# Kernel tuning notes

Hardware: AMD Instinct MI355X
Metric: run time of the kernel (lower is better)

Reference implementation:

```python
import jax, jax.numpy as jnp
import numpy as np

B, T, H = 4, 2048, 1024
NH, NKV, HD = 16, 4, 64  # heads, kv heads, head_dim

def setup_inputs() -> dict:
    key = jax.random.key(0)
    ks = jax.random.split(key, 5)
    s = 0.02
    return {
        "x": jax.random.normal(ks[0], (B, T, H), dtype=jnp.float32),
        "wq": jax.random.normal(ks[1], (H, NH * HD), dtype=jnp.float32) * s,
        "wk": jax.random.normal(ks[2], (H, NKV * HD), dtype=jnp.float32) * s,
        "wv": jax.random.normal(ks[3], (H, NKV * HD), dtype=jnp.float32) * s,
        "wo": jax.random.normal(ks[4], (NH * HD, H), dtype=jnp.float32) * s,
    }

def reference(x, wq, wk, wv, wo):
    b, t, _ = x.shape
    q = (x @ wq).reshape(b, t, NH, HD).transpose(0, 2, 1, 3)    # [B,NH,T,HD]
    k = (x @ wk).reshape(b, t, NKV, HD).transpose(0, 2, 1, 3)   # [B,NKV,T,HD]
    v = (x @ wv).reshape(b, t, NKV, HD).transpose(0, 2, 1, 3)
    n_rep = NH // NKV
    # repeat_kv: expand each kv head n_rep times along the head axis
    k_rep = jnp.repeat(k, n_rep, axis=1)                        # [B,NH,T,HD]
    v_rep = jnp.repeat(v, n_rep, axis=1)
    scale = 1.0 / np.sqrt(HD).astype(np.float32)
    scores = jnp.einsum('bhqd,bhkd->bhqk', q, k_rep) * scale    # [B,NH,T,T]
    key_pos = jnp.arange(t)[None, :]
    q_pos = jnp.arange(t)[:, None]  # past_len = 0 (no kv cache)
    causal = key_pos > q_pos                                    # [T,T]
    scores = jnp.where(causal[None, None], -jnp.inf, scores)
    probs = jax.nn.softmax(scores, axis=-1)                     # dropout is identity (eval / rate 0)
    attn = jnp.einsum('bhqk,bhkd->bhqd', probs, v_rep)          # [B,NH,T,HD]
    attn = attn.transpose(0, 2, 1, 3).reshape(b, t, NH * HD)
    return attn @ wo
```

## Files before the change

### kernel.cpp

```cpp
#include <hip/hip_runtime.h>
#include <hip/hip_bf16.h>

using bf16 = __hip_bfloat16;
typedef __attribute__((ext_vector_type(8))) short bf16x8;
typedef __attribute__((ext_vector_type(4))) short bf16x4;
typedef __attribute__((ext_vector_type(4))) float f32x4;

typedef const __attribute__((address_space(1))) void* as1_t;
typedef __attribute__((address_space(3))) void* as3_t;
__device__ __forceinline__ void load_lds16(const void* g, void* l) {
    __builtin_amdgcn_global_load_lds((as1_t)g, (as3_t)l, 16, 0, 0);
}

#if !__has_builtin(__builtin_amdgcn_exp2f)
extern "C" __device__ float __ocml_native_exp2_f32(float);
#endif
__device__ __forceinline__ float exp2_fast(float x) {
#if __has_builtin(__builtin_amdgcn_exp2f)
    return __builtin_amdgcn_exp2f(x);
#else
    return __ocml_native_exp2_f32(x);
#endif
}

__global__ __launch_bounds__(256) void cast_f32_bf16(const float* __restrict__ src,
                                                     bf16* __restrict__ dst, int n4) {
    int i = (blockIdx.x * 256 + threadIdx.x);
    if (i >= n4) return;
    const float4 v = *(const float4*)(src + (long)i * 4);
    bf16 t[4];
    t[0] = __float2bfloat16(v.x);
    t[1] = __float2bfloat16(v.y);
    t[2] = __float2bfloat16(v.z);
    t[3] = __float2bfloat16(v.w);
    *(uint2*)(dst + (long)i * 4) = *(uint2*)t;
}

__global__ __launch_bounds__(256) void transpose_cast4(const float* __restrict__ wq,
                                                       const float* __restrict__ wk,
                                                       const float* __restrict__ wv,
                                                       const float* __restrict__ wo,
                                                       bf16* __restrict__ wqkvT,
                                                       bf16* __restrict__ woT) {
    __shared__ float tile[32][33];
    const int bx = blockIdx.x;
    const int k0 = blockIdx.y * 32;
    const float* src; bf16* dst; int N, n0;
    if (bx < 32)      { src = wq; dst = wqkvT;              N = 1024; n0 = bx * 32; }
    else if (bx < 40) { src = wk; dst = wqkvT + 1024*1024;  N = 256;  n0 = (bx - 32) * 32; }
    else if (bx < 48) { src = wv; dst = wqkvT + 1280*1024;  N = 256;  n0 = (bx - 40) * 32; }
    else              { src = wo; dst = woT;                N = 1024; n0 = (bx - 48) * 32; }
    const int tx = threadIdx.x & 31;
    const int ty = threadIdx.x >> 5;
    for (int i = 0; i < 32; i += 8)
        tile[ty + i][tx] = src[(long)(k0 + ty + i) * N + n0 + tx];
    __syncthreads();
    for (int i = 0; i < 32; i += 8)
        dst[(long)(n0 + ty + i) * 1024 + k0 + tx] = __float2bfloat16(tile[tx][ty + i]);
}

__global__ __launch_bounds__(256) void transpose_v(const bf16* __restrict__ qkv,
                                                   bf16* __restrict__ vt) {
    __shared__ bf16 tile[64][72];
    const int tb = blockIdx.x, kvh = blockIdx.y, b = blockIdx.z;
    const int r = threadIdx.x >> 3;
    const int c = (threadIdx.x & 7) * 8;
    const bf16* src = qkv + (long)(b * 2048 + tb * 64) * 1536 + 1280 + kvh * 64;
    *(uint4*)&tile[r][c]      = *(const uint4*)(src + (long)r * 1536 + c);
    *(uint4*)&tile[r + 32][c] = *(const uint4*)(src + (long)(r + 32) * 1536 + c);
    __syncthreads();
    bf16* dst = vt + (long)(b * 4 + kvh) * 64 * 2048 + tb * 64;
#pragma unroll
    for (int rr = 0; rr < 2; rr++) {
        const int d = r + rr * 32;
        bf16 t8[8];
#pragma unroll
        for (int e = 0; e < 8; e++) t8[e] = tile[c + e][d];
        *(uint4*)(dst + (long)d * 2048 + c) = *(uint4*)t8;
    }
}

template <bool BF16_OUT>
__global__ __launch_bounds__(256) void gemm_bt(const bf16* __restrict__ A,
                                               const bf16* __restrict__ Bt,
                                               void* __restrict__ C,
                                               int M, int N, int K) {
    __shared__ bf16 Ash[128 * 64];
    __shared__ bf16 Bsh[128 * 64];
    const int tid  = threadIdx.x;
    const int lane = tid & 63;
    const int wid  = tid >> 6;
    const int wm   = (wid >> 1) * 64;
    const int wn   = (wid & 1) * 64;
    const int quad = lane >> 4;
    const int l16  = lane & 15;

    const int nbn = N >> 7;
    const int nwg = (M >> 7) * nbn;
    const int per = nwg >> 3;
    const int wg  = blockIdx.x;
    const int swz = (wg & 7) * per + (wg >> 3);
    const int bm  = swz / nbn;
    const int bn  = swz - bm * nbn;

    const int rS  = tid >> 3;
    const int chS = tid & 7;
    const int gch = (chS ^ (rS & 7)) * 8;

    const bf16* pa = A  + (long)(bm * 128 + rS) * K + gch;
    const bf16* pb = Bt + (long)(bn * 128 + rS) * K + gch;
    bf16* laB = Ash + (wid << 9);
    bf16* lbB = Bsh + (wid << 9);

    f32x4 acc[4][4] = {};

    for (int k0 = 0; k0 < K; k0 += 64) {
        __syncthreads();
#pragma unroll
        for (int m = 0; m < 4; m++) {
            load_lds16(pa + k0 + (long)(32 * m) * K, laB + m * 2048);
            load_lds16(pb + k0 + (long)(32 * m) * K, lbB + m * 2048);
        }
        __syncthreads();

#pragma unroll
        for (int kf = 0; kf < 2; kf++) {
            const int sw = ((kf * 4 + quad) ^ (l16 & 7)) * 8;
            bf16x8 af[4], bfr[4];
#pragma unroll
            for (int i = 0; i < 4; i++) af[i]  = *(const bf16x8*)&Ash[(wm + i * 16 + l16) * 64 + sw];
#pragma unroll
            for (int j = 0; j < 4; j++) bfr[j] = *(const bf16x8*)&Bsh[(wn + j * 16 + l16) * 64 + sw];
#pragma unroll
            for (int i = 0; i < 4; i++)
#pragma unroll
                for (int j = 0; j < 4; j++)
                    acc[i][j] = __builtin_amdgcn_mfma_f32_16x16x32_bf16(af[i], bfr[j], acc[i][j], 0, 0, 0);
        }
    }

#pragma unroll
    for (int i = 0; i < 4; i++) {
#pragma unroll
        for (int r = 0; r < 4; r++) {
            const long row = (long)(bm * 128 + wm + i * 16 + quad * 4 + r);
#pragma unroll
            for (int j = 0; j < 4; j++) {
                const int col = bn * 128 + wn + j * 16 + l16;
                const float v = acc[i][j][r];
                if (BF16_OUT) ((bf16*)C)[row * N + col] = __float2bfloat16(v);
                else          ((float*)C)[row * N + col] = v;
            }
        }
    }
}

__global__ __launch_bounds__(256) void attn_kernel(const bf16* __restrict__ qkv,
                                                   const bf16* __restrict__ vt,
                                                   bf16* __restrict__ attn) {
    __shared__ bf16 Ksh[2][64 * 64];
    __shared__ bf16 Vsh[2][64 * 64];

    const int tid  = threadIdx.x;
    const int lane = tid & 63;
    const int wid  = tid >> 6;
    const int quad = lane >> 4;
    const int l16  = lane & 15;
    const int h    = blockIdx.y;
    const int b    = blockIdx.z;
    const int kvh  = h >> 2;
    const int pb   = blockIdx.x;

    const float ls = 0.125f * 1.44269504f;

    bf16x4 ones;
    { short o1 = (short)0x3F80; short t4[4] = {o1, o1, o1, o1}; ones = *(const bf16x4*)t4; }

    const bf16* kg = qkv + (long)(b * 2048) * 1536 + 1024 + kvh * 64;
    const bf16* vg = vt + (long)(b * 4 + kvh) * 64 * 2048;
    const int r0 = tid >> 3;
    const int ch0 = tid & 7;
    const int c0 = ch0 * 8;

    const bf16* kp0 = kg + (long)r0 * 1536 + c0;
    const bf16* kp1 = kp0 + (long)32 * 1536;
    const bf16* vp0 = vg + (long)r0 * 2048 + c0;
    const bf16* vp1 = vp0 + (long)32 * 2048;

    const int wo0 = r0 * 64 + ((ch0 ^ (r0 & 7)) * 8);
    const int wo1 = wo0 + 32 * 64;
    const int kchunkA = (quad ^ (l16 & 7)) * 8;
    const int kchunkB = ((4 + quad) ^ (l16 & 7)) * 8;
    const int vsub    = (quad & 1) * 4;
    const int vq      = quad >> 1;

#pragma unroll 1
    for (int seg = 0; seg < 2; ++seg) {
        const int qb     = seg ? pb : (31 - pb);
        const int qblock = qb * 64;
        const int q0     = qblock + wid * 16;

        const bf16* qbase = qkv + (long)(b * 2048 + q0 + l16) * 1536 + h * 64;
        bf16x8 qf[2];
#pragma unroll
        for (int kf = 0; kf < 2; kf++) {
            const bf16* qp = qbase + kf * 32 + quad * 8;
            bf16 t8[8];
#pragma unroll
            for (int e = 0; e < 8; e++) t8[e] = __float2bfloat16(__bfloat162float(qp[e]) * ls);
            qf[kf] = *(const bf16x8*)t8;
        }

        f32x4 o[4] = {};
        f32x4 ol = {};

        uint4 kr0 = *(const uint4*)kp0;
        uint4 kr1 = *(const uint4*)kp1;
        uint4 vr0 = *(const uint4*)vp0;
        uint4 vr1 = *(const uint4*)vp1;

        __syncthreads();

        const int nIter = qb + 1;
        for (int it = 0; it < nIter; ++it) {
            bf16* __restrict__ Kb = &Ksh[it & 1][0];
            bf16* __restrict__ Vb = &Vsh[it & 1][0];
            *(uint4*)&Kb[wo0] = kr0;
            *(uint4*)&Kb[wo1] = kr1;
            *(uint4*)&Vb[wo0] = vr0;
            *(uint4*)&Vb[wo1] = vr1;
            __syncthreads();

            if (it + 1 < nIter) {
                const long ko = (long)(it + 1) * 64 * 1536;
                const long vo = (it + 1) * 64;
                kr0 = *(const uint4*)(kp0 + ko);
                kr1 = *(const uint4*)(kp1 + ko);
                vr0 = *(const uint4*)(vp0 + vo);
                vr1 = *(const uint4*)(vp1 + vo);
            }

            f32x4 s[4] = {};
            __builtin_amdgcn_s_setprio(1);
#pragma unroll
            for (int kvt = 0; kvt < 4; kvt++)
#pragma unroll
                for (int kf = 0; kf < 2; kf++) {
                    const int rbase = (kvt * 16 + l16) * 64;
                    const bf16x8 kfr = *(const bf16x8*)&Kb[rbase + (kf ? kchunkB : kchunkA)];
                    s[kvt] = __builtin_amdgcn_mfma_f32_16x16x32_bf16(kfr, qf[kf], s[kvt], 0, 0, 0);
                }
            __builtin_amdgcn_s_setprio(0);

            if (it == nIter - 1) {
                const int qq = wid * 16 + l16;
#pragma unroll
                for (int kvt = 0; kvt < 4; kvt++)
#pragma unroll
                    for (int r = 0; r < 4; r++)
                        if (kvt * 16 + quad * 4 + r > qq) s[kvt][r] = -1e30f;
            }

#pragma unroll
            for (int kvt = 0; kvt < 4; kvt++) {
                float2 p01, p23;
                p01.x = exp2_fast(s[kvt][0]);
                p01.y = exp2_fast(s[kvt][1]);
                p23.x = exp2_fast(s[kvt][2]);
                p23.y = exp2_fast(s[kvt][3]);
                __hip_bfloat162 pk01 = __float22bfloat162_rn(p01);
                __hip_bfloat162 pk23 = __float22bfloat162_rn(p23);
                bf16x4 pk;
                *(__hip_bfloat162*)&pk       = pk01;
                *((__hip_bfloat162*)&pk + 1) = pk23;

                __builtin_amdgcn_s_setprio(1);
                ol = __builtin_amdgcn_mfma_f32_16x16x16bf16_1k(ones, pk, ol, 0, 0, 0);
#pragma unroll
                for (int dt = 0; dt < 4; dt++) {
                    const int vaddr = (dt * 16 + l16) * 64 +
                                      (((kvt * 2 + vq) ^ (l16 & 7)) * 8) + vsub;
                    const bf16x4 vf = *(const bf16x4*)&Vb[vaddr];
                    o[dt] = __builtin_amdgcn_mfma_f32_16x16x16bf16_1k(vf, pk, o[dt], 0, 0, 0);
                }
                __builtin_amdgcn_s_setprio(0);
            }
        }

        const float inv = 1.f / ol[0];
        bf16* obase = attn + (long)(b * 2048 + q0 + l16) * 1024 + h * 64;
#pragma unroll
        for (int dt = 0; dt < 4; dt++) {
            bf16 t4[4];
#pragma unroll
            for (int r = 0; r < 4; r++) t4[r] = __float2bfloat16(o[dt][r] * inv);
            *(uint2*)(obase + dt * 16 + quad * 4) = *(uint2*)t4;
        }
    }
}

extern "C" void kernel_launch(void* const* d_in, const int* in_sizes, int n_in,
                              void* d_out, int out_size, void* d_ws, size_t ws_size,
                              hipStream_t stream) {
    const float* x  = (const float*)d_in[0];
    const float* wq = (const float*)d_in[1];
    const float* wk = (const float*)d_in[2];
    const float* wv = (const float*)d_in[3];
    const float* wo = (const float*)d_in[4];
    float* out = (float*)d_out;

    char* ws = (char*)d_ws;
    bf16* xb     = (bf16*)(ws);
    bf16* wqkvT  = (bf16*)(ws + 16777216);
    bf16* woT    = (bf16*)(ws + 19922944);
    bf16* qkv    = (bf16*)(ws + 22020096);
    bf16* vt     = (bf16*)(ws + 47185920);
    bf16* attn   = (bf16*)(ws + 51380224);

    cast_f32_bf16<<<8192, 256, 0, stream>>>(x, xb, 2097152);

    transpose_cast4<<<dim3(80, 32), 256, 0, stream>>>(wq, wk, wv, wo, wqkvT, woT);

    gemm_bt<true><<<768, 256, 0, stream>>>(xb, wqkvT, qkv, 8192, 1536, 1024);

    transpose_v<<<dim3(32, 4, 4), 256, 0, stream>>>(qkv, vt);

    attn_kernel<<<dim3(16, 16, 4), 256, 0, stream>>>(qkv, vt, attn);

    gemm_bt<false><<<512, 256, 0, stream>>>(attn, woT, out, 8192, 1024, 1024);
}
```

Baseline: 208.1 us.

## Fuse prolog cast kernels and double-buffer B tile in GEMM

The x cast and weight transpose-cast kernels become one launch, with block ranges dispatching to each job. In the GEMM, the B tile is now double-buffered in LDS so the next B tile's load overlaps the current MFMA work. The A tile stays single-buffered and is reloaded after a barrier. This adds LDS use and an extra barrier per iteration, and the A load stays exposed.

```diff
diff --git a/kernel.cpp b/kernel.cpp
--- a/kernel.cpp
+++ b/kernel.cpp
@@ -23,28 +23,30 @@
 #endif
 }
 
-__global__ __launch_bounds__(256) void cast_f32_bf16(const float* __restrict__ src,
-                                                     bf16* __restrict__ dst, int n4) {
-    int i = (blockIdx.x * 256 + threadIdx.x);
-    if (i >= n4) return;
-    const float4 v = *(const float4*)(src + (long)i * 4);
-    bf16 t[4];
-    t[0] = __float2bfloat16(v.x);
-    t[1] = __float2bfloat16(v.y);
-    t[2] = __float2bfloat16(v.z);
-    t[3] = __float2bfloat16(v.w);
-    *(uint2*)(dst + (long)i * 4) = *(uint2*)t;
-}
-
-__global__ __launch_bounds__(256) void transpose_cast4(const float* __restrict__ wq,
-                                                       const float* __restrict__ wk,
-                                                       const float* __restrict__ wv,
-                                                       const float* __restrict__ wo,
-                                                       bf16* __restrict__ wqkvT,
-                                                       bf16* __restrict__ woT) {
+__global__ __launch_bounds__(256) void prolog_kernel(const float* __restrict__ x,
+                                                     const float* __restrict__ wq,
+                                                     const float* __restrict__ wk,
+                                                     const float* __restrict__ wv,
+                                                     const float* __restrict__ wo,
+                                                     bf16* __restrict__ xb,
+                                                     bf16* __restrict__ wqkvT,
+                                                     bf16* __restrict__ woT) {
     __shared__ float tile[32][33];
-    const int bx = blockIdx.x;
-    const int k0 = blockIdx.y * 32;
+    const int bxg = blockIdx.x;
+    if (bxg < 8192) {
+        const int i = bxg * 256 + threadIdx.x;
+        const float4 v = *(const float4*)(x + (long)i * 4);
+        bf16 t[4];
+        t[0] = __float2bfloat16(v.x);
+        t[1] = __float2bfloat16(v.y);
+        t[2] = __float2bfloat16(v.z);
+        t[3] = __float2bfloat16(v.w);
+        *(uint2*)(xb + (long)i * 4) = *(uint2*)t;
+        return;
+    }
+    const int tcb = bxg - 8192;
+    const int bx  = tcb >> 5;
+    const int k0  = (tcb & 31) * 32;
     const float* src; bf16* dst; int N, n0;
     if (bx < 32)      { src = wq; dst = wqkvT;              N = 1024; n0 = bx * 32; }
     else if (bx < 40) { src = wk; dst = wqkvT + 1024*1024;  N = 256;  n0 = (bx - 32) * 32; }
@@ -86,7 +88,7 @@
                                                void* __restrict__ C,
                                                int M, int N, int K) {
     __shared__ bf16 Ash[128 * 64];
-    __shared__ bf16 Bsh[128 * 64];
+    __shared__ bf16 Bsh[2][128 * 64];
     const int tid  = threadIdx.x;
     const int lane = tid & 63;
     const int wid  = tid >> 6;
@@ -109,20 +111,29 @@
 
     const bf16* pa = A  + (long)(bm * 128 + rS) * K + gch;
     const bf16* pb = Bt + (long)(bn * 128 + rS) * K + gch;
-    bf16* laB = Ash + (wid << 9);
-    bf16* lbB = Bsh + (wid << 9);
+    const int ldsOff = wid << 9;
+    bf16* laB = Ash + ldsOff;
 
     f32x4 acc[4][4] = {};
-
-    for (int k0 = 0; k0 < K; k0 += 64) {
-        __syncthreads();
-#pragma unroll
-        for (int m = 0; m < 4; m++) {
-            load_lds16(pa + k0 + (long)(32 * m) * K, laB + m * 2048);
-            load_lds16(pb + k0 + (long)(32 * m) * K, lbB + m * 2048);
-        }
-        __syncthreads();
-
+    const int nt = K >> 6;
+
+#pragma unroll
+    for (int m = 0; m < 4; m++) {
+        load_lds16(pa + (long)(32 * m) * K, laB + m * 2048);
+        load_lds16(pb + (long)(32 * m) * K, &Bsh[0][ldsOff + m * 2048]);
+    }
+    __syncthreads();
+
+    for (int t = 0; t < nt; ++t) {
+        const int cur = t & 1;
+        if (t + 1 < nt) {
+            const long ko = (long)(t + 1) * 64;
+#pragma unroll
+            for (int m = 0; m < 4; m++)
+                load_lds16(pb + ko + (long)(32 * m) * K, &Bsh[cur ^ 1][ldsOff + m * 2048]);
+        }
+
+        const bf16* __restrict__ Bb = &Bsh[cur][0];
 #pragma unroll
         for (int kf = 0; kf < 2; kf++) {
             const int sw = ((kf * 4 + quad) ^ (l16 & 7)) * 8;
@@ -130,13 +141,22 @@
 #pragma unroll
             for (int i = 0; i < 4; i++) af[i]  = *(const bf16x8*)&Ash[(wm + i * 16 + l16) * 64 + sw];
 #pragma unroll
-            for (int j = 0; j < 4; j++) bfr[j] = *(const bf16x8*)&Bsh[(wn + j * 16 + l16) * 64 + sw];
+            for (int j = 0; j < 4; j++) bfr[j] = *(const bf16x8*)&Bb[(wn + j * 16 + l16) * 64 + sw];
 #pragma unroll
             for (int i = 0; i < 4; i++)
 #pragma unroll
                 for (int j = 0; j < 4; j++)
                     acc[i][j] = __builtin_amdgcn_mfma_f32_16x16x32_bf16(af[i], bfr[j], acc[i][j], 0, 0, 0);
         }
+        __syncthreads();
+
+        if (t + 1 < nt) {
+            const long ko = (long)(t + 1) * 64;
+#pragma unroll
+            for (int m = 0; m < 4; m++)
+                load_lds16(pa + ko + (long)(32 * m) * K, laB + m * 2048);
+        }
+        __syncthreads();
     }
 
 #pragma unroll
@@ -317,9 +337,7 @@
     bf16* vt     = (bf16*)(ws + 47185920);
     bf16* attn   = (bf16*)(ws + 51380224);
 
-    cast_f32_bf16<<<8192, 256, 0, stream>>>(x, xb, 2097152);
-
-    transpose_cast4<<<dim3(80, 32), 256, 0, stream>>>(wq, wk, wv, wo, wqkvT, woT);
+    prolog_kernel<<<10752, 256, 0, stream>>>(x, wq, wk, wv, wo, xb, wqkvT, woT);
 
     gemm_bt<true><<<768, 256, 0, stream>>>(xb, wqkvT, qkv, 8192, 1536, 1024);
 
```

Result: no change. 208.1 us (-0.0%).

## Merge prolog casts into one launch and fuse V transpose into QKV GEMM epilogue

Applied to the files above, without the earlier changes.

The x cast and the weight transpose-casts now run in a single kernel with a flattened grid. The separate V transpose kernel is removed: QKV GEMM blocks covering the V columns write their tile transposed straight into the vt buffer. This drops two kernel launches and one extra read/write pass over V. The cost is scattered 8-byte transposed stores in the GEMM epilogue, and qkv no longer holds the V columns.

```diff
diff --git a/kernel.cpp b/kernel.cpp
--- a/kernel.cpp
+++ b/kernel.cpp
@@ -23,28 +23,30 @@
 #endif
 }
 
-__global__ __launch_bounds__(256) void cast_f32_bf16(const float* __restrict__ src,
-                                                     bf16* __restrict__ dst, int n4) {
-    int i = (blockIdx.x * 256 + threadIdx.x);
-    if (i >= n4) return;
-    const float4 v = *(const float4*)(src + (long)i * 4);
-    bf16 t[4];
-    t[0] = __float2bfloat16(v.x);
-    t[1] = __float2bfloat16(v.y);
-    t[2] = __float2bfloat16(v.z);
-    t[3] = __float2bfloat16(v.w);
-    *(uint2*)(dst + (long)i * 4) = *(uint2*)t;
-}
-
-__global__ __launch_bounds__(256) void transpose_cast4(const float* __restrict__ wq,
-                                                       const float* __restrict__ wk,
-                                                       const float* __restrict__ wv,
-                                                       const float* __restrict__ wo,
-                                                       bf16* __restrict__ wqkvT,
-                                                       bf16* __restrict__ woT) {
+__global__ __launch_bounds__(256) void prolog_kernel(const float* __restrict__ x,
+                                                     const float* __restrict__ wq,
+                                                     const float* __restrict__ wk,
+                                                     const float* __restrict__ wv,
+                                                     const float* __restrict__ wo,
+                                                     bf16* __restrict__ xb,
+                                                     bf16* __restrict__ wqkvT,
+                                                     bf16* __restrict__ woT) {
     __shared__ float tile[32][33];
-    const int bx = blockIdx.x;
-    const int k0 = blockIdx.y * 32;
+    const int bxg = blockIdx.x;
+    if (bxg < 8192) {
+        const int i = bxg * 256 + threadIdx.x;
+        const float4 v = *(const float4*)(x + (long)i * 4);
+        bf16 t[4];
+        t[0] = __float2bfloat16(v.x);
+        t[1] = __float2bfloat16(v.y);
+        t[2] = __float2bfloat16(v.z);
+        t[3] = __float2bfloat16(v.w);
+        *(uint2*)(xb + (long)i * 4) = *(uint2*)t;
+        return;
+    }
+    const int tcb = bxg - 8192;
+    const int bx  = tcb >> 5;
+    const int k0  = (tcb & 31) * 32;
     const float* src; bf16* dst; int N, n0;
     if (bx < 32)      { src = wq; dst = wqkvT;              N = 1024; n0 = bx * 32; }
     else if (bx < 40) { src = wk; dst = wqkvT + 1024*1024;  N = 256;  n0 = (bx - 32) * 32; }
@@ -59,31 +61,11 @@
         dst[(long)(n0 + ty + i) * 1024 + k0 + tx] = __float2bfloat16(tile[tx][ty + i]);
 }
 
-__global__ __launch_bounds__(256) void transpose_v(const bf16* __restrict__ qkv,
-                                                   bf16* __restrict__ vt) {
-    __shared__ bf16 tile[64][72];
-    const int tb = blockIdx.x, kvh = blockIdx.y, b = blockIdx.z;
-    const int r = threadIdx.x >> 3;
-    const int c = (threadIdx.x & 7) * 8;
-    const bf16* src = qkv + (long)(b * 2048 + tb * 64) * 1536 + 1280 + kvh * 64;
-    *(uint4*)&tile[r][c]      = *(const uint4*)(src + (long)r * 1536 + c);
-    *(uint4*)&tile[r + 32][c] = *(const uint4*)(src + (long)(r + 32) * 1536 + c);
-    __syncthreads();
-    bf16* dst = vt + (long)(b * 4 + kvh) * 64 * 2048 + tb * 64;
-#pragma unroll
-    for (int rr = 0; rr < 2; rr++) {
-        const int d = r + rr * 32;
-        bf16 t8[8];
-#pragma unroll
-        for (int e = 0; e < 8; e++) t8[e] = tile[c + e][d];
-        *(uint4*)(dst + (long)d * 2048 + c) = *(uint4*)t8;
-    }
-}
-
-template <bool BF16_OUT>
+template <bool BF16_OUT, bool V_SPLIT>
 __global__ __launch_bounds__(256) void gemm_bt(const bf16* __restrict__ A,
                                                const bf16* __restrict__ Bt,
                                                void* __restrict__ C,
+                                               bf16* __restrict__ vt,
                                                int M, int N, int K) {
     __shared__ bf16 Ash[128 * 64];
     __shared__ bf16 Bsh[128 * 64];
@@ -137,6 +119,26 @@
                 for (int j = 0; j < 4; j++)
                     acc[i][j] = __builtin_amdgcn_mfma_f32_16x16x32_bf16(af[i], bfr[j], acc[i][j], 0, 0, 0);
         }
+    }
+
+    if (V_SPLIT && bn >= 10) {
+        const int kvh = (bn - 10) * 2 + (wn >> 6);
+        const int bq  = bm >> 4;
+        const int t0b = (bm & 15) * 128 + wm;
+        bf16* vbase = vt + ((long)(bq * 4 + kvh) * 64) * 2048;
+#pragma unroll
+        for (int i = 0; i < 4; i++) {
+#pragma unroll
+            for (int j = 0; j < 4; j++) {
+                const int d  = j * 16 + l16;
+                const int t0 = t0b + i * 16 + quad * 4;
+                bf16 t4[4];
+#pragma unroll
+                for (int r = 0; r < 4; r++) t4[r] = __float2bfloat16(acc[i][j][r]);
+                *(uint2*)(vbase + (long)d * 2048 + t0) = *(uint2*)t4;
+            }
+        }
+        return;
     }
 
 #pragma unroll
@@ -317,15 +319,11 @@
     bf16* vt     = (bf16*)(ws + 47185920);
     bf16* attn   = (bf16*)(ws + 51380224);
 
-    cast_f32_bf16<<<8192, 256, 0, stream>>>(x, xb, 2097152);
-
-    transpose_cast4<<<dim3(80, 32), 256, 0, stream>>>(wq, wk, wv, wo, wqkvT, woT);
-
-    gemm_bt<true><<<768, 256, 0, stream>>>(xb, wqkvT, qkv, 8192, 1536, 1024);
-
-    transpose_v<<<dim3(32, 4, 4), 256, 0, stream>>>(qkv, vt);
+    prolog_kernel<<<10752, 256, 0, stream>>>(x, wq, wk, wv, wo, xb, wqkvT, woT);
+
+    gemm_bt<true, true><<<768, 256, 0, stream>>>(xb, wqkvT, qkv, vt, 8192, 1536, 1024);
 
     attn_kernel<<<dim3(16, 16, 4), 256, 0, stream>>>(qkv, vt, attn);
 
-    gemm_bt<false><<<512, 256, 0, stream>>>(attn, woT, out, 8192, 1024, 1024);
-}
+    gemm_bt<false, false><<<512, 256, 0, stream>>>(attn, woT, out, nullptr, 8192, 1024, 1024);
+}
```

New measurement: 206.4 us (median of 2 runs). Within noise of the previous version (-0.8%).
